# Optimization experiments

Hardware: AMD Instinct MI355X
Metric: run time of the kernel (lower is better)

The kernel has to match this reference:

```python
import jax, jax.numpy as jnp
import numpy as np


def setup_inputs() -> dict:
    key = jax.random.key(0)
    k1, k2 = jax.random.split(key)
    n_task, shot, feat, n_class = 32, 2048, 1024, 512
    inputs = jax.random.normal(k1, (n_task, shot, feat), dtype=jnp.float32)
    weights = jax.random.normal(k2, (n_task, n_class, feat), dtype=jnp.float32)
    return {"inputs": inputs, "weights": weights, "temp": 15}


def reference(inputs, weights, temp):
    # logits[t,s,c] = temp * (x.w - 0.5*||w||^2 - 0.5*||x||^2)
    dots = jnp.einsum('tsf,tcf->tsc', inputs, weights)        # [T,S,C]
    w_sq = 0.5 * jnp.sum(weights * weights, axis=2)           # [T,C]
    x_sq = 0.5 * jnp.sum(inputs * inputs, axis=2)             # [T,S]
    logits = temp * (dots - w_sq[:, None, :] - x_sq[:, :, None])
    return jnp.argmax(logits, axis=2)                         # [T,S] int
```

## Files before the change

### kernel.cpp

```cpp
#include <hip/hip_runtime.h>
#include <cstdint>
#include <cstddef>

#define T_TASKS 32
#define S_SHOT  2048
#define F_FEAT  1024
#define C_CLS   512
#define MARGIN  0.1f

typedef _Float16 f16;
typedef _Float16 f16x4 __attribute__((ext_vector_type(4)));
typedef _Float16 f16x8 __attribute__((ext_vector_type(8)));
typedef float    f32x4 __attribute__((ext_vector_type(4)));

__device__ __forceinline__ void gl_lds16(const void* g, void* l) {
  auto gp = (const __attribute__((address_space(1))) uint32_t*)(g);
  auto lp = (__attribute__((address_space(3))) uint32_t*)(l);
  __builtin_amdgcn_global_load_lds(gp, lp, 16, 0, 0);
}

__device__ __forceinline__ void upd3(float v, int i,
                                     float& v1, int& i1,
                                     float& v2, int& i2,
                                     float& v3, int& i3) {
  if (v > v1 || (v == v1 && i < i1)) { v3=v2; i3=i2; v2=v1; i2=i1; v1=v; i1=i; }
  else if (v > v2 || (v == v2 && i < i2)) { v3=v2; i3=i2; v2=v; i2=i; }
  else if (v > v3 || (v == v3 && i < i3)) { v3=v; i3=i; }
}

__global__ __launch_bounds__(256) void prep_w(const float* __restrict__ W,
                                              f16* __restrict__ Wh,
                                              float* __restrict__ wsq) {
  int rid = blockIdx.x * 4 + (threadIdx.x >> 6);
  int ln  = threadIdx.x & 63;
  int c   = rid & (C_CLS - 1);
  int t   = rid >> 9;
  const float* wr = W + (size_t)rid * F_FEAT;
  double s = 0.0;
#pragma unroll
  for (int j = 0; j < 4; ++j) {
    int f = (j * 64 + ln) * 4;
    float4 v = *(const float4*)(wr + f);
    s += (double)v.x * v.x + (double)v.y * v.y +
         (double)v.z * v.z + (double)v.w * v.w;
    f16x4 h;
    h.x = (f16)v.x; h.y = (f16)v.y; h.z = (f16)v.z; h.w = (f16)v.w;
    int kt = f >> 5;
    int q  = (f >> 3) & 3;
    int jj = f & 7;
    int u  = c * 4 + ((q + (c >> 1)) & 3);
    size_t off = ((size_t)(t * 32 + kt) << 14) + (size_t)u * 8 + jj;
    *(f16x4*)(Wh + off) = h;
  }
#pragma unroll
  for (int off = 32; off > 0; off >>= 1) s += __shfl_xor(s, off);
  if (ln == 0) wsq[rid] = (float)(0.5 * s);
}

__global__ __launch_bounds__(256, 2) void gemm_argmax(
    const float* __restrict__ X, const float* __restrict__ W,
    const f16* __restrict__ Wh, const float* __restrict__ wsq,
    int* __restrict__ out) {
  __shared__ __align__(16) f16 sWh[16384];
  __shared__ __align__(16) f16 sXh[64 * 40];
  __shared__ __align__(16) f16 sXl[64 * 40];
  __shared__ float swsq[C_CLS];
  __shared__ float cv[64][2][3];
  __shared__ int   ci[64][2][3];
  __shared__ int   amb_cnt;
  __shared__ int   amb_list[64];

  const int tid = threadIdx.x;
  const int wv  = tid >> 6, ln = tid & 63;
  const int rg  = wv >> 1, cg = wv & 1;
  const int m   = ln & 15, q = ln >> 4;
  const int bx  = blockIdx.x;
  const int t   = bx >> 5, rb = bx & 31;
  const int row0 = rb * 64;

  swsq[tid]       = wsq[t * C_CLS + tid];
  swsq[tid + 256] = wsq[t * C_CLS + tid + 256];
  if (tid == 0) amb_cnt = 0;

  const f32x4 zero4 = {0.f, 0.f, 0.f, 0.f};
  f32x4 acc[2][16];
#pragma unroll
  for (int a = 0; a < 2; ++a)
#pragma unroll
    for (int b = 0; b < 16; ++b) acc[a][b] = zero4;

  const float* Xblk = X + ((size_t)t * S_SHOT + row0) * F_FEAT;
  const f16*   Wht  = Wh + ((size_t)(t * 32) << 14);

  f16* aph = sXh + (rg * 32 + m) * 40 + q * 8;
  f16* apl = sXl + (rg * 32 + m) * 40 + q * 8;
  const int c0 = cg * 256 + m;
  const int u0 = c0 * 4 + ((q + (c0 >> 1)) & 3);
  const f16* bp = sWh + u0 * 8;

  for (int kt = 0; kt < 32; ++kt) {
    const f16* gW = Wht + (kt << 14) + wv * 4096 + ln * 8;
    f16* lW = sWh + wv * 4096;
#pragma unroll
    for (int i = 0; i < 8; ++i) gl_lds16(gW + i * 512, lW + i * 512);

#pragma unroll
    for (int j = 0; j < 2; ++j) {
      int idx = tid + j * 256;
      int r = idx >> 3, q4 = idx & 7;
      float4 v = *(const float4*)(Xblk + (size_t)r * F_FEAT + kt * 32 + q4 * 4);
      f16x4 h, l;
      h.x = (f16)v.x; l.x = (f16)(v.x - (float)h.x);
      h.y = (f16)v.y; l.y = (f16)(v.y - (float)h.y);
      h.z = (f16)v.z; l.z = (f16)(v.z - (float)h.z);
      h.w = (f16)v.w; l.w = (f16)(v.w - (float)h.w);
      *(f16x4*)(sXh + r * 40 + q4 * 4) = h;
      *(f16x4*)(sXl + r * 40 + q4 * 4) = l;
    }
    __syncthreads();

    f16x8 ah0 = *(const f16x8*)(aph);
    f16x8 ah1 = *(const f16x8*)(aph + 16 * 40);
    f16x8 al0 = *(const f16x8*)(apl);
    f16x8 al1 = *(const f16x8*)(apl + 16 * 40);
#pragma unroll
    for (int ct = 0; ct < 16; ++ct) {
      f16x8 bh = *(const f16x8*)(bp + ct * 512);
      acc[0][ct] = __builtin_amdgcn_mfma_f32_16x16x32_f16(ah0, bh, acc[0][ct], 0, 0, 0);
      acc[0][ct] = __builtin_amdgcn_mfma_f32_16x16x32_f16(al0, bh, acc[0][ct], 0, 0, 0);
      acc[1][ct] = __builtin_amdgcn_mfma_f32_16x16x32_f16(ah1, bh, acc[1][ct], 0, 0, 0);
      acc[1][ct] = __builtin_amdgcn_mfma_f32_16x16x32_f16(al1, bh, acc[1][ct], 0, 0, 0);
    }
    __syncthreads();
  }

#pragma unroll
  for (int rt = 0; rt < 2; ++rt) {
#pragma unroll
    for (int rr = 0; rr < 4; ++rr) {
      float v1 = -3.4e38f, v2 = -3.4e38f, v3 = -3.4e38f;
      int   i1 = 0x7fffffff, i2 = 0x7fffffff, i3 = 0x7fffffff;
#pragma unroll
      for (int ct = 0; ct < 16; ++ct) {
        int cidx = c0 + ct * 16;
        float sc = acc[rt][ct][rr] - swsq[cidx];
        upd3(sc, cidx, v1, i1, v2, i2, v3, i3);
      }
      for (int off = 1; off < 16; off <<= 1) {
        float w1 = __shfl_xor(v1, off); int j1 = __shfl_xor(i1, off);
        float w2 = __shfl_xor(v2, off); int j2 = __shfl_xor(i2, off);
        float w3 = __shfl_xor(v3, off); int j3 = __shfl_xor(i3, off);
        upd3(w1, j1, v1, i1, v2, i2, v3, i3);
        upd3(w2, j2, v1, i1, v2, i2, v3, i3);
        upd3(w3, j3, v1, i1, v2, i2, v3, i3);
      }
      if (m == 0) {
        int row = rg * 32 + rt * 16 + q * 4 + rr;
        cv[row][cg][0] = v1; ci[row][cg][0] = i1;
        cv[row][cg][1] = v2; ci[row][cg][1] = i2;
        cv[row][cg][2] = v3; ci[row][cg][2] = i3;
      }
    }
  }
  __syncthreads();

  if (tid < 64) {
    float a1 = cv[tid][0][0]; int aj = ci[tid][0][0];
    float b1 = cv[tid][1][0]; int bj = ci[tid][1][0];
    float win, runner; int widx;
    if (a1 > b1 || (a1 == b1 && aj < bj)) {
      win = a1; widx = aj; runner = fmaxf(b1, cv[tid][0][1]);
    } else {
      win = b1; widx = bj; runner = fmaxf(a1, cv[tid][1][1]);
    }
    if (win - runner >= MARGIN) {
      out[t * S_SHOT + row0 + tid] = widx;
    } else {
      int p = atomicAdd(&amb_cnt, 1);
      amb_list[p] = tid;
    }
  }
  __syncthreads();

  int nA = amb_cnt;
  for (int a = wv; a < nA; a += 4) {
    int rl = amb_list[a];
    const float* xr = X + ((size_t)t * S_SHOT + row0 + rl) * F_FEAT;
    double best = -1.0e300; int bidx = 0x7fffffff;
    for (int g = 0; g < 2; ++g) {
      for (int k = 0; k < 3; ++k) {
        int cidx = ci[rl][g][k];
        const float* wr = W + ((size_t)t * C_CLS + cidx) * F_FEAT;
        double sd = 0.0, sw = 0.0;
        for (int j = 0; j < 16; ++j) {
          float xv = xr[ln + 64 * j];
          float wv2 = wr[ln + 64 * j];
          sd += (double)xv * (double)wv2;
          sw += (double)wv2 * (double)wv2;
        }
#pragma unroll
        for (int off = 32; off > 0; off >>= 1) {
          sd += __shfl_xor(sd, off);
          sw += __shfl_xor(sw, off);
        }
        double sc = sd - 0.5 * sw;
        if (sc > best || (sc == best && cidx < bidx)) { best = sc; bidx = cidx; }
      }
    }
    if (ln == 0) out[t * S_SHOT + row0 + rl] = bidx;
  }
}

extern "C" void kernel_launch(void* const* d_in, const int* in_sizes, int n_in,
                              void* d_out, int out_size, void* d_ws, size_t ws_size,
                              hipStream_t stream) {
  (void)in_sizes; (void)n_in; (void)out_size;
  const float* X = (const float*)d_in[0];
  const float* W = (const float*)d_in[1];
  const size_t wh_bytes = (size_t)T_TASKS * C_CLS * F_FEAT * sizeof(f16);
  const size_t need = wh_bytes + (size_t)T_TASKS * C_CLS * sizeof(float);
  if (ws_size < need) return;
  f16*   Wh  = (f16*)d_ws;
  float* wsq = (float*)((char*)d_ws + wh_bytes);
  int*   out = (int*)d_out;
  prep_w<<<T_TASKS * C_CLS / 4, 256, 0, stream>>>(W, Wh, wsq);
  gemm_argmax<<<T_TASKS * (S_SHOT / 64), 256, 0, stream>>>(X, W, Wh, wsq, out);
}
```

Measured before the change: 958.0 us.

## Double-buffer W tiles and prefetch X to overlap loads with MFMA

Adds a second LDS buffer for the fp16 W tile and issues the next k-tile's global-to-LDS W loads and X register loads before running the current tile's MFMAs, so memory latency overlaps compute. Shared memory is placed in a union so the epilogue arrays reuse the main-loop space, keeping occupancy despite the extra buffer. It also remaps block indices across XCDs, raises wave priority during MFMA, and splits the ambiguous-row fp64 recheck so each (row, candidate) pair is handled by a separate wave. The cost is more LDS per block and manual waitcnt/barrier handling that has to be correct.

```diff
diff --git a/kernel.cpp b/kernel.cpp
--- a/kernel.cpp
+++ b/kernel.cpp
@@ -7,6 +7,7 @@
 #define F_FEAT  1024
 #define C_CLS   512
 #define MARGIN  0.1f
+#define NBLK    (T_TASKS * (S_SHOT / 64))
 
 typedef _Float16 f16;
 typedef _Float16 f16x4 __attribute__((ext_vector_type(4)));
@@ -57,30 +58,76 @@
   if (ln == 0) wsq[rid] = (float)(0.5 * s);
 }
 
+struct MainSh {
+  f16 W0[16384];
+  f16 W1[16384];
+  f16 Xh[64 * 40];
+  f16 Xl[64 * 40];
+};
+struct EpiSh {
+  float  swsq[C_CLS];
+  float  cv[64][2][3];
+  int    ci[64][2][3];
+  double rs[48];
+  int    amb_cnt;
+  int    amb_list[64];
+};
+union ShU { MainSh m; EpiSh e; };
+
+__device__ __forceinline__ void issue_w8(const f16* Wht, f16* dst, int ktn,
+                                         int wv, int ln) {
+  const f16* g = Wht + ((size_t)ktn << 14) + wv * 4096 + ln * 8;
+  f16* l = dst + wv * 4096;
+#pragma unroll
+  for (int i = 0; i < 8; ++i) gl_lds16(g + i * 512, l + i * 512);
+}
+
+__device__ __forceinline__ void cvt_write_x(float4 a, float4 b,
+                                            f16* xwh, f16* xwl) {
+  f16x4 h, l;
+  h.x = (f16)a.x; l.x = (f16)(a.x - (float)h.x);
+  h.y = (f16)a.y; l.y = (f16)(a.y - (float)h.y);
+  h.z = (f16)a.z; l.z = (f16)(a.z - (float)h.z);
+  h.w = (f16)a.w; l.w = (f16)(a.w - (float)h.w);
+  *(f16x4*)(xwh) = h;
+  *(f16x4*)(xwl) = l;
+  h.x = (f16)b.x; l.x = (f16)(b.x - (float)h.x);
+  h.y = (f16)b.y; l.y = (f16)(b.y - (float)h.y);
+  h.z = (f16)b.z; l.z = (f16)(b.z - (float)h.z);
+  h.w = (f16)b.w; l.w = (f16)(b.w - (float)h.w);
+  *(f16x4*)(xwh + 32 * 40) = h;
+  *(f16x4*)(xwl + 32 * 40) = l;
+}
+
 __global__ __launch_bounds__(256, 2) void gemm_argmax(
     const float* __restrict__ X, const float* __restrict__ W,
     const f16* __restrict__ Wh, const float* __restrict__ wsq,
     int* __restrict__ out) {
-  __shared__ __align__(16) f16 sWh[16384];
-  __shared__ __align__(16) f16 sXh[64 * 40];
-  __shared__ __align__(16) f16 sXl[64 * 40];
-  __shared__ float swsq[C_CLS];
-  __shared__ float cv[64][2][3];
-  __shared__ int   ci[64][2][3];
-  __shared__ int   amb_cnt;
-  __shared__ int   amb_list[64];
+  __shared__ __align__(16) ShU sh;
 
   const int tid = threadIdx.x;
   const int wv  = tid >> 6, ln = tid & 63;
   const int rg  = wv >> 1, cg = wv & 1;
   const int m   = ln & 15, q = ln >> 4;
-  const int bx  = blockIdx.x;
-  const int t   = bx >> 5, rb = bx & 31;
+
+  int bx = blockIdx.x;
+  bx = (bx & 7) * (NBLK / 8) + (bx >> 3);
+  const int t    = bx >> 5, rb = bx & 31;
   const int row0 = rb * 64;
 
-  swsq[tid]       = wsq[t * C_CLS + tid];
-  swsq[tid + 256] = wsq[t * C_CLS + tid + 256];
-  if (tid == 0) amb_cnt = 0;
+  const float* Xblk = X + ((size_t)t * S_SHOT + row0) * F_FEAT;
+  const f16*   Wht  = Wh + ((size_t)(t * 32) << 14);
+
+  const int sr = tid >> 3, sq = tid & 7;
+  const float* xg0 = Xblk + (size_t)sr * F_FEAT + sq * 4;
+  const float* xg1 = xg0 + (size_t)32 * F_FEAT;
+  f16* xwh = sh.m.Xh + sr * 40 + sq * 4;
+  f16* xwl = sh.m.Xl + sr * 40 + sq * 4;
+
+  const f16* aph = sh.m.Xh + (rg * 32 + m) * 40 + q * 8;
+  const f16* apl = sh.m.Xl + (rg * 32 + m) * 40 + q * 8;
+  const int c0 = cg * 256 + m;
+  const int u0 = c0 * 4 + ((q + (c0 >> 1)) & 3);
 
   const f32x4 zero4 = {0.f, 0.f, 0.f, 0.f};
   f32x4 acc[2][16];
@@ -89,40 +136,37 @@
 #pragma unroll
     for (int b = 0; b < 16; ++b) acc[a][b] = zero4;
 
-  const float* Xblk = X + ((size_t)t * S_SHOT + row0) * F_FEAT;
-  const f16*   Wht  = Wh + ((size_t)(t * 32) << 14);
-
-  f16* aph = sXh + (rg * 32 + m) * 40 + q * 8;
-  f16* apl = sXl + (rg * 32 + m) * 40 + q * 8;
-  const int c0 = cg * 256 + m;
-  const int u0 = c0 * 4 + ((q + (c0 >> 1)) & 3);
-  const f16* bp = sWh + u0 * 8;
-
+  f16* Wr = sh.m.W0;
+  f16* Ws = sh.m.W1;
+
+  {
+    float4 a = *(const float4*)(xg0);
+    float4 b = *(const float4*)(xg1);
+    issue_w8(Wht, Wr, 0, wv, ln);
+    cvt_write_x(a, b, xwh, xwl);
+    asm volatile("s_waitcnt vmcnt(0)" ::: "memory");
+    asm volatile("s_waitcnt lgkmcnt(0)" ::: "memory");
+    __builtin_amdgcn_s_barrier();
+  }
+
+#pragma unroll 1
   for (int kt = 0; kt < 32; ++kt) {
-    const f16* gW = Wht + (kt << 14) + wv * 4096 + ln * 8;
-    f16* lW = sWh + wv * 4096;
-#pragma unroll
-    for (int i = 0; i < 8; ++i) gl_lds16(gW + i * 512, lW + i * 512);
-
-#pragma unroll
-    for (int j = 0; j < 2; ++j) {
-      int idx = tid + j * 256;
-      int r = idx >> 3, q4 = idx & 7;
-      float4 v = *(const float4*)(Xblk + (size_t)r * F_FEAT + kt * 32 + q4 * 4);
-      f16x4 h, l;
-      h.x = (f16)v.x; l.x = (f16)(v.x - (float)h.x);
-      h.y = (f16)v.y; l.y = (f16)(v.y - (float)h.y);
-      h.z = (f16)v.z; l.z = (f16)(v.z - (float)h.z);
-      h.w = (f16)v.w; l.w = (f16)(v.w - (float)h.w);
-      *(f16x4*)(sXh + r * 40 + q4 * 4) = h;
-      *(f16x4*)(sXl + r * 40 + q4 * 4) = l;
-    }
-    __syncthreads();
-
+    const bool more = (kt < 31);
+    float4 a, b;
+    if (more) {
+      a = *(const float4*)(xg0 + (kt + 1) * 32);
+      b = *(const float4*)(xg1 + (kt + 1) * 32);
+      issue_w8(Wht, Ws, kt + 1, wv, ln);
+    }
     f16x8 ah0 = *(const f16x8*)(aph);
     f16x8 ah1 = *(const f16x8*)(aph + 16 * 40);
     f16x8 al0 = *(const f16x8*)(apl);
     f16x8 al1 = *(const f16x8*)(apl + 16 * 40);
+    asm volatile("s_waitcnt lgkmcnt(0)" ::: "memory");
+    __builtin_amdgcn_s_barrier();
+
+    __builtin_amdgcn_s_setprio(1);
+    const f16* bp = Wr + u0 * 8;
 #pragma unroll
     for (int ct = 0; ct < 16; ++ct) {
       f16x8 bh = *(const f16x8*)(bp + ct * 512);
@@ -131,8 +175,20 @@
       acc[1][ct] = __builtin_amdgcn_mfma_f32_16x16x32_f16(ah1, bh, acc[1][ct], 0, 0, 0);
       acc[1][ct] = __builtin_amdgcn_mfma_f32_16x16x32_f16(al1, bh, acc[1][ct], 0, 0, 0);
     }
-    __syncthreads();
-  }
+    __builtin_amdgcn_s_setprio(0);
+
+    if (more) cvt_write_x(a, b, xwh, xwl);
+    asm volatile("s_waitcnt vmcnt(0)" ::: "memory");
+    asm volatile("s_waitcnt lgkmcnt(0)" ::: "memory");
+    __builtin_amdgcn_s_barrier();
+    f16* tmp = Wr; Wr = Ws; Ws = tmp;
+  }
+  __syncthreads();
+
+  sh.e.swsq[tid]       = wsq[t * C_CLS + tid];
+  sh.e.swsq[tid + 256] = wsq[t * C_CLS + tid + 256];
+  if (tid == 0) sh.e.amb_cnt = 0;
+  __syncthreads();
 
 #pragma unroll
   for (int rt = 0; rt < 2; ++rt) {
@@ -143,7 +199,7 @@
 #pragma unroll
       for (int ct = 0; ct < 16; ++ct) {
         int cidx = c0 + ct * 16;
-        float sc = acc[rt][ct][rr] - swsq[cidx];
+        float sc = acc[rt][ct][rr] - sh.e.swsq[cidx];
         upd3(sc, cidx, v1, i1, v2, i2, v3, i3);
       }
       for (int off = 1; off < 16; off <<= 1) {
@@ -156,58 +212,74 @@
       }
       if (m == 0) {
         int row = rg * 32 + rt * 16 + q * 4 + rr;
-        cv[row][cg][0] = v1; ci[row][cg][0] = i1;
-        cv[row][cg][1] = v2; ci[row][cg][1] = i2;
-        cv[row][cg][2] = v3; ci[row][cg][2] = i3;
+        sh.e.cv[row][cg][0] = v1; sh.e.ci[row][cg][0] = i1;
+        sh.e.cv[row][cg][1] = v2; sh.e.ci[row][cg][1] = i2;
+        sh.e.cv[row][cg][2] = v3; sh.e.ci[row][cg][2] = i3;
       }
     }
   }
   __syncthreads();
 
   if (tid < 64) {
-    float a1 = cv[tid][0][0]; int aj = ci[tid][0][0];
-    float b1 = cv[tid][1][0]; int bj = ci[tid][1][0];
+    float a1 = sh.e.cv[tid][0][0]; int aj = sh.e.ci[tid][0][0];
+    float b1 = sh.e.cv[tid][1][0]; int bj = sh.e.ci[tid][1][0];
     float win, runner; int widx;
     if (a1 > b1 || (a1 == b1 && aj < bj)) {
-      win = a1; widx = aj; runner = fmaxf(b1, cv[tid][0][1]);
+      win = a1; widx = aj; runner = fmaxf(b1, sh.e.cv[tid][0][1]);
     } else {
-      win = b1; widx = bj; runner = fmaxf(a1, cv[tid][1][1]);
+      win = b1; widx = bj; runner = fmaxf(a1, sh.e.cv[tid][1][1]);
     }
     if (win - runner >= MARGIN) {
       out[t * S_SHOT + row0 + tid] = widx;
     } else {
-      int p = atomicAdd(&amb_cnt, 1);
-      amb_list[p] = tid;
+      int p = atomicAdd(&sh.e.amb_cnt, 1);
+      sh.e.amb_list[p] = tid;
     }
   }
   __syncthreads();
 
-  int nA = amb_cnt;
-  for (int a = wv; a < nA; a += 4) {
-    int rl = amb_list[a];
-    const float* xr = X + ((size_t)t * S_SHOT + row0 + rl) * F_FEAT;
-    double best = -1.0e300; int bidx = 0x7fffffff;
-    for (int g = 0; g < 2; ++g) {
-      for (int k = 0; k < 3; ++k) {
-        int cidx = ci[rl][g][k];
-        const float* wr = W + ((size_t)t * C_CLS + cidx) * F_FEAT;
-        double sd = 0.0, sw = 0.0;
-        for (int j = 0; j < 16; ++j) {
-          float xv = xr[ln + 64 * j];
-          float wv2 = wr[ln + 64 * j];
-          sd += (double)xv * (double)wv2;
-          sw += (double)wv2 * (double)wv2;
-        }
-#pragma unroll
-        for (int off = 32; off > 0; off >>= 1) {
-          sd += __shfl_xor(sd, off);
-          sw += __shfl_xor(sw, off);
-        }
-        double sc = sd - 0.5 * sw;
+  int nA = sh.e.amb_cnt;
+  for (int base = 0; base < nA; base += 8) {
+    int nr = nA - base; if (nr > 8) nr = 8;
+    int np = nr * 6;
+    for (int p = wv; p < np; p += 4) {
+      int rrow = p / 6;
+      int cand = p - rrow * 6;
+      int rl   = sh.e.amb_list[base + rrow];
+      int g    = (cand >= 3) ? 1 : 0;
+      int k    = cand - g * 3;
+      int cidx = sh.e.ci[rl][g][k];
+      const float* xr = X + ((size_t)t * S_SHOT + row0 + rl) * F_FEAT;
+      const float* wr = W + ((size_t)t * C_CLS + cidx) * F_FEAT;
+      double sd = 0.0, sw = 0.0;
+#pragma unroll
+      for (int j = 0; j < 16; ++j) {
+        float xv  = xr[ln + 64 * j];
+        float wv2 = wr[ln + 64 * j];
+        sd += (double)xv * (double)wv2;
+        sw += (double)wv2 * (double)wv2;
+      }
+#pragma unroll
+      for (int off = 32; off > 0; off >>= 1) {
+        sd += __shfl_xor(sd, off);
+        sw += __shfl_xor(sw, off);
+      }
+      if (ln == 0) sh.e.rs[p] = sd - 0.5 * sw;
+    }
+    __syncthreads();
+    if (tid < nr) {
+      int rl = sh.e.amb_list[base + tid];
+      double best = -1.0e300; int bidx = 0x7fffffff;
+#pragma unroll
+      for (int cand = 0; cand < 6; ++cand) {
+        int g = cand / 3, k = cand % 3;
+        int cidx = sh.e.ci[rl][g][k];
+        double sc = sh.e.rs[tid * 6 + cand];
         if (sc > best || (sc == best && cidx < bidx)) { best = sc; bidx = cidx; }
       }
-    }
-    if (ln == 0) out[t * S_SHOT + row0 + rl] = bidx;
+      out[t * S_SHOT + row0 + rl] = bidx;
+    }
+    __syncthreads();
   }
 }
 
@@ -224,5 +296,5 @@
   float* wsq = (float*)((char*)d_ws + wh_bytes);
   int*   out = (int*)d_out;
   prep_w<<<T_TASKS * C_CLS / 4, 256, 0, stream>>>(W, Wh, wsq);
-  gemm_argmax<<<T_TASKS * (S_SHOT / 64), 256, 0, stream>>>(X, W, Wh, wsq, out);
-}
+  gemm_argmax<<<NBLK, 256, 0, stream>>>(X, W, Wh, wsq, out);
+}
```

Measured after the change: 793.5 us. 1.21x faster.
